# Performance work log

Hardware: AMD Instinct MI355X
Metric: run time of the kernel (lower is better)

Reference implementation:

```python
import jax, jax.numpy as jnp
import numpy as np
import math

B, N, D_IN, D, D_OUT, H = 4, 2048, 128, 128, 256, 4  # D = dim_hidden//2


def _lin(key, din, dout):
    k1, k2 = jax.random.split(key)
    s = 1.0 / math.sqrt(din)
    W = jax.random.uniform(k1, (din, dout), jnp.float32, -s, s)
    b = jax.random.uniform(k2, (dout,), jnp.float32, -s, s)
    return W, b


def setup_inputs() -> dict:
    key = jax.random.key(0)
    ks = jax.random.split(key, 20)
    inp = {"X": jax.random.normal(ks[0], (B, N, D_IN), jnp.float32)}
    # mab dims: (dim_Q, dim_K) -> dim_V=D for each of the 3 MABs
    mab_dims = [(D_IN, D_IN), (D, D), (D, D)]
    ki = 1
    for i, (dq, dk) in enumerate(mab_dims):
        inp[f"m{i}_Wq"], inp[f"m{i}_bq"] = _lin(ks[ki], dq, D); ki += 1
        inp[f"m{i}_Wk"], inp[f"m{i}_bk"] = _lin(ks[ki], dk, D); ki += 1
        inp[f"m{i}_Wv"], inp[f"m{i}_bv"] = _lin(ks[ki], dk, D); ki += 1
        inp[f"m{i}_Wo"], inp[f"m{i}_bo"] = _lin(ks[ki], D, D); ki += 1
    a = math.sqrt(6.0 / (D + 1))  # xavier_uniform for S [1,1,D]
    inp["S"] = jax.random.uniform(ks[ki], (1, 1, D), jnp.float32, -a, a); ki += 1
    inp["pW"], inp["pb"] = _lin(ks[ki], D, D_OUT)
    return inp


def _mab(Q, K, Wq, bq, Wk, bk, Wv, bv, Wo, bo):
    # Linear projections
    Qp = Q @ Wq + bq                       # [B, Nq, D]
    Kp = K @ Wk + bk                       # [B, Nk, D]
    Vp = K @ Wv + bv                       # [B, Nk, D]
    b, nq, dV = Qp.shape
    dh = dV // H
    # torch split(dim_split,2)+cat(0) == head-split on last dim
    Qh = Qp.reshape(b, nq, H, dh)
    Kh = Kp.reshape(b, -1, H, dh)
    Vh = Vp.reshape(b, -1, H, dh)
    # sigmoid attention (no softmax normalizer)
    A = jax.nn.sigmoid(jnp.einsum('bnhd,bmhd->bhnm', Qh, Kh) / jnp.sqrt(jnp.float32(dV)))
    O = Qh + jnp.einsum('bhnm,bmhd->bnhd', A, Vh)
    O = O.reshape(b, nq, dV)
    # residual ReLU-FFN (no LayerNorm since ln=False)
    return O + jax.nn.relu(O @ Wo + bo)


def reference(X,
              m0_Wq, m0_bq, m0_Wk, m0_bk, m0_Wv, m0_bv, m0_Wo, m0_bo,
              m1_Wq, m1_bq, m1_Wk, m1_bk, m1_Wv, m1_bv, m1_Wo, m1_bo,
              m2_Wq, m2_bq, m2_Wk, m2_bk, m2_Wv, m2_bv, m2_Wo, m2_bo,
              S, pW, pb):
    # SAB layer 0: self-attention, dim_in -> D
    Xh = _mab(X, X, m0_Wq, m0_bq, m0_Wk, m0_bk, m0_Wv, m0_bv, m0_Wo, m0_bo)
    # SAB layer 1: D -> D
    Xh = _mab(Xh, Xh, m1_Wq, m1_bq, m1_Wk, m1_bk, m1_Wv, m1_bv, m1_Wo, m1_bo)
    # PMA pooling: seed queries attend over the set
    Sb = jnp.broadcast_to(S, (Xh.shape[0], S.shape[1], S.shape[2]))
    P = _mab(Sb, Xh, m2_Wq, m2_bq, m2_Wk, m2_bk, m2_Wv, m2_bv, m2_Wo, m2_bo)
    # final projection D -> dim_hidden
    return P @ pW + pb  # [B, num_seeds, D_OUT]
```

## Files before the change

kernel.cpp:

```cpp
#include <hip/hip_runtime.h>
#include <hip/hip_bf16.h>

typedef __hip_bfloat16 HB;
typedef __attribute__((ext_vector_type(8))) short short8;
typedef __attribute__((ext_vector_type(4))) short short4v;
typedef __attribute__((ext_vector_type(4))) float f32x4;
typedef __attribute__((ext_vector_type(2))) unsigned int uint2v;
typedef __attribute__((ext_vector_type(4))) unsigned int uint4v;

constexpr int Bn = 4, Nn = 2048, Dm = 128, Hh = 4;
constexpr int MN = Bn * Nn;
constexpr size_t SZ = (size_t)MN * Dm;

static __device__ __forceinline__ short f2bs(float x) {
    __hip_bfloat16 h = __float2bfloat16(x);
    return __builtin_bit_cast(short, h);
}
static __device__ __forceinline__ unsigned short f2bh(float x) {
    return (unsigned short)((__builtin_bit_cast(unsigned int, x) + 0x8000u) >> 16);
}
static __device__ __forceinline__ unsigned int pk2(float lo, float hi) {
    unsigned int a = __builtin_bit_cast(unsigned int, lo) + 0x8000u;
    unsigned int b = __builtin_bit_cast(unsigned int, hi) + 0x8000u;
#if __has_builtin(__builtin_amdgcn_perm)
    return __builtin_amdgcn_perm(b, a, 0x07060302u);
#else
    return (a >> 16) | (b & 0xFFFF0000u);
#endif
}

__global__ void k_wprep(const float* __restrict__ Wa, const float* __restrict__ Wb,
                        const float* __restrict__ Wc, const float* __restrict__ Wd,
                        const float* __restrict__ We, const float* __restrict__ Wf,
                        const float* __restrict__ Wg, const float* __restrict__ Wh,
                        const float* __restrict__ Wi, const float* __restrict__ Wj,
                        HB* __restrict__ WtAll) {
    const float* src;
    switch (blockIdx.x) {
        case 0: src = Wa; break; case 1: src = Wb; break;
        case 2: src = Wc; break; case 3: src = Wd; break;
        case 4: src = We; break; case 5: src = Wf; break;
        case 6: src = Wg; break; case 7: src = Wh; break;
        case 8: src = Wi; break; default: src = Wj; break;
    }
    HB* dst = WtAll + (size_t)blockIdx.x * 16384;
    #pragma unroll
    for (int it = 0; it < 8; ++it) {
        int idx = it * 256 + threadIdx.x;
        int g = idx >> 7, c = idx & 127;
        short8 p;
        #pragma unroll
        for (int j = 0; j < 8; ++j) p[j] = f2bs(src[(size_t)(g * 8 + j) * 128 + c]);
        *(short8*)((short*)dst + (size_t)idx * 8) = p;
    }
}

template<int NW, int RELU, int NEXTRA, int FUSE>
__global__ __launch_bounds__(512) void k_linm(
        const float* __restrict__ A, const float* __restrict__ extra,
        const HB* __restrict__ Wt0, const float* __restrict__ b0,
        const HB* __restrict__ Wt1, const float* __restrict__ b1,
        const HB* __restrict__ Wt2, const float* __restrict__ b2,
        float* __restrict__ C0, float* __restrict__ C1,
        HB* __restrict__ Kb, HB* __restrict__ Vt) {
    const int tid = threadIdx.x;
    const int w = tid >> 6, lane = tid & 63, l15 = lane & 15, quad = lane >> 4;
    const int row0 = blockIdx.x * 32 + (w >> 2) * 16;
    const int cbase = (w & 3) * 32;

    short8 af[4];
    #pragma unroll
    for (int kc = 0; kc < 4; ++kc) {
        const float* ap = A + (size_t)(row0 + l15) * 128 + kc * 32 + quad * 8;
        float4 x0 = *(const float4*)ap;
        float4 x1 = *(const float4*)(ap + 4);
        if (NEXTRA) {
            const float* ep = extra + (size_t)(row0 + l15) * 128 + kc * 32 + quad * 8;
            float4 e0 = *(const float4*)ep, e1 = *(const float4*)(ep + 4);
            x0.x += e0.x; x0.y += e0.y; x0.z += e0.z; x0.w += e0.w;
            x1.x += e1.x; x1.y += e1.y; x1.z += e1.z; x1.w += e1.w;
        }
        uint4v u;
        u[0] = pk2(x0.x, x0.y); u[1] = pk2(x0.z, x0.w);
        u[2] = pk2(x1.x, x1.y); u[3] = pk2(x1.z, x1.w);
        af[kc] = __builtin_bit_cast(short8, u);
    }

    f32x4 zero = {0.f, 0.f, 0.f, 0.f};
    #pragma unroll
    for (int ct = 0; ct < 2; ++ct) {
        const int col = cbase + ct * 16 + l15;
        #pragma unroll
        for (int s = 0; s < NW; ++s) {
            const HB* Wt = (s == 0) ? Wt0 : (s == 1) ? Wt1 : Wt2;
            const float* bs = (s == 0) ? b0 : (s == 1) ? b1 : b2;
            f32x4 acc = zero;
            #pragma unroll
            for (int kc = 0; kc < 4; ++kc) {
                short8 bf = *(const short8*)((const short*)Wt + ((size_t)(kc * 4 + quad) * 128 + col) * 8);
                acc = __builtin_amdgcn_mfma_f32_16x16x32_bf16(af[kc], bf, acc, 0, 0, 0);
            }
            float bb = bs[col];
            if (s == 0 || !FUSE) {
                float* Cs = (s == 0) ? C0 : C1;
                #pragma unroll
                for (int r = 0; r < 4; ++r) {
                    int row = row0 + quad * 4 + r;
                    float v = acc[r] + bb;
                    if (RELU && s == 0) {
                        float st = A[(size_t)row * 128 + col];
                        if (NEXTRA) st += extra[(size_t)row * 128 + col];
                        v = fmaxf(v, 0.f) + st;
                    }
                    Cs[(size_t)row * 128 + col] = v;
                }
            } else if (s == 1) {
                #pragma unroll
                for (int r = 0; r < 4; ++r) {
                    int row = row0 + quad * 4 + r;
                    ((unsigned short*)Kb)[(size_t)row * 128 + col] = f2bh(acc[r] + bb);
                }
            } else {
                int b_ = row0 >> 11;
                int mloc = (row0 + quad * 4) & 2047;
                int slotb = (mloc & ~31) + (((mloc & 15) >> 2) << 3) + (((mloc >> 4) & 1) << 2);
                int h_ = col >> 5, dh = col & 31;
                uint2v pv;
                pv[0] = pk2(acc[0] + bb, acc[1] + bb);
                pv[1] = pk2(acc[2] + bb, acc[3] + bb);
                *(short4v*)((short*)Vt + ((size_t)((b_ * 4 + h_) * 32 + dh)) * 2048 + slotb)
                    = __builtin_bit_cast(short4v, pv);
            }
        }
    }
}

__global__ __launch_bounds__(256) void k_attn3(const float* __restrict__ Qp, const HB* __restrict__ Kbf,
                                               const HB* __restrict__ Vt, float* __restrict__ Opart) {
    const int tid = threadIdx.x;
    const int w = tid >> 6, lane = tid & 63, l15 = lane & 15, quad = lane >> 4;
    const int bh = blockIdx.x >> 6, qg = blockIdx.x & 63;
    const int b = bh >> 2, h = bh & 3;

    __shared__ float ldsacc[4][32][36];

    const float nscale = -0.08838834764831845f;

    short8 aq[2];
    #pragma unroll
    for (int qa = 0; qa < 2; ++qa) {
        const float* qp = Qp + (size_t)(b * Nn + qg * 32 + qa * 16 + l15) * 128 + h * 32 + quad * 8;
        float4 q0 = *(const float4*)qp;
        float4 q1 = *(const float4*)(qp + 4);
        uint4v u;
        u[0] = pk2(q0.x, q0.y); u[1] = pk2(q0.z, q0.w);
        u[2] = pk2(q1.x, q1.y); u[3] = pk2(q1.z, q1.w);
        aq[qa] = __builtin_bit_cast(short8, u);
    }

    f32x4 zero = {0.f, 0.f, 0.f, 0.f};
    f32x4 o[2][2];
    o[0][0] = zero; o[0][1] = zero; o[1][0] = zero; o[1][1] = zero;

    const short* Kb = (const short*)Kbf + (size_t)b * Nn * 128 + h * 32;
    const short* Vb = (const short*)Vt + (size_t)bh * 32 * Nn;

    #pragma unroll 2
    for (int m0 = w * 512; m0 < w * 512 + 512; m0 += 64) {
        short8 kb[4];
        #pragma unroll
        for (int mc = 0; mc < 4; ++mc)
            kb[mc] = *(const short8*)(Kb + (size_t)(m0 + mc * 16 + l15) * 128 + quad * 8);
        short8 vf[2][2];
        #pragma unroll
        for (int t = 0; t < 2; ++t)
            #pragma unroll
            for (int u = 0; u < 2; ++u)
                vf[t][u] = *(const short8*)(Vb + (size_t)(t * 16 + l15) * Nn + m0 + u * 32 + quad * 8);

        #pragma unroll
        for (int qa = 0; qa < 2; ++qa) {
            f32x4 s[4];
            #pragma unroll
            for (int mc = 0; mc < 4; ++mc)
                s[mc] = __builtin_amdgcn_mfma_f32_16x16x32_bf16(kb[mc], aq[qa], zero, 0, 0, 0);
            #pragma unroll
            for (int u = 0; u < 2; ++u) {
                f32x4 lo = s[2 * u], hi = s[2 * u + 1];
                float p0 = __builtin_amdgcn_rcpf(1.f + __expf(lo[0] * nscale));
                float p1 = __builtin_amdgcn_rcpf(1.f + __expf(lo[1] * nscale));
                float p2 = __builtin_amdgcn_rcpf(1.f + __expf(lo[2] * nscale));
                float p3 = __builtin_amdgcn_rcpf(1.f + __expf(lo[3] * nscale));
                float p4 = __builtin_amdgcn_rcpf(1.f + __expf(hi[0] * nscale));
                float p5 = __builtin_amdgcn_rcpf(1.f + __expf(hi[1] * nscale));
                float p6 = __builtin_amdgcn_rcpf(1.f + __expf(hi[2] * nscale));
                float p7 = __builtin_amdgcn_rcpf(1.f + __expf(hi[3] * nscale));
                uint4v pu;
                pu[0] = pk2(p0, p1); pu[1] = pk2(p2, p3);
                pu[2] = pk2(p4, p5); pu[3] = pk2(p6, p7);
                short8 pf = __builtin_bit_cast(short8, pu);
                #pragma unroll
                for (int t = 0; t < 2; ++t)
                    o[qa][t] = __builtin_amdgcn_mfma_f32_16x16x32_bf16(vf[t][u], pf, o[qa][t], 0, 0, 0);
            }
        }
    }

    #pragma unroll
    for (int qa = 0; qa < 2; ++qa)
        #pragma unroll
        for (int t = 0; t < 2; ++t)
            *(f32x4*)&ldsacc[w][qa * 16 + l15][t * 16 + quad * 4] = o[qa][t];
    __syncthreads();
    const int row = tid >> 3, cc = (tid & 7) * 4;
    f32x4 r0 = *(f32x4*)&ldsacc[0][row][cc];
    f32x4 r1 = *(f32x4*)&ldsacc[1][row][cc];
    f32x4 r2 = *(f32x4*)&ldsacc[2][row][cc];
    f32x4 r3 = *(f32x4*)&ldsacc[3][row][cc];
    f32x4 sum = (r0 + r1) + (r2 + r3);
    *(f32x4*)(Opart + (size_t)(b * Nn + qg * 32 + row) * 128 + h * 32 + cc) = sum;
}

__global__ void k_pma2(const float* __restrict__ S, const float* __restrict__ Wq, const float* __restrict__ bq,
                       const float* __restrict__ Kp, const float* __restrict__ Vp,
                       float* __restrict__ P0part) {
    const int bh = blockIdx.x, b = bh >> 2, h = bh & 3;
    const int ms = blockIdx.y;
    const int tid = threadIdx.x;
    __shared__ float4 qs4[8];
    float* qs = (float*)qs4;
    if (tid < 32) {
        float a = bq[h * 32 + tid];
        for (int k = 0; k < 128; ++k)
            a = fmaf(S[k], Wq[k * Dm + h * 32 + tid], a);
        qs[tid] = a;
    }
    __syncthreads();

    float4 q[8];
    #pragma unroll
    for (int i = 0; i < 8; ++i) q[i] = qs4[i];

    const size_t base = (size_t)b * Nn * Dm + h * 32;
    const float nscale = -0.08838834764831845f;
    const int m = ms * 256 + tid;

    const float4* kp = (const float4*)(Kp + base + (size_t)m * Dm);
    const float4* vp = (const float4*)(Vp + base + (size_t)m * Dm);
    float d0 = 0.f, d1 = 0.f, d2 = 0.f, d3 = 0.f;
    #pragma unroll
    for (int c = 0; c < 8; c += 4) {
        float4 k0 = kp[c+0], k1 = kp[c+1], k2 = kp[c+2], k3 = kp[c+3];
        d0 += q[c+0].x*k0.x + q[c+0].y*k0.y + q[c+0].z*k0.z + q[c+0].w*k0.w;
        d1 += q[c+1].x*k1.x + q[c+1].y*k1.y + q[c+1].z*k1.z + q[c+1].w*k1.w;
        d2 += q[c+2].x*k2.x + q[c+2].y*k2.y + q[c+2].z*k2.z + q[c+2].w*k2.w;
        d3 += q[c+3].x*k3.x + q[c+3].y*k3.y + q[c+3].z*k3.z + q[c+3].w*k3.w;
    }
    float dot = (d0 + d1) + (d2 + d3);
    float a = __builtin_amdgcn_rcpf(1.f + __expf(dot * nscale));
    float4 acc[8];
    #pragma unroll
    for (int c = 0; c < 8; ++c) {
        float4 vv = vp[c];
        acc[c].x = a * vv.x; acc[c].y = a * vv.y; acc[c].z = a * vv.z; acc[c].w = a * vv.w;
    }
    #pragma unroll
    for (int off = 1; off < 64; off <<= 1) {
        #pragma unroll
        for (int c = 0; c < 8; ++c) {
            acc[c].x += __shfl_xor(acc[c].x, off);
            acc[c].y += __shfl_xor(acc[c].y, off);
            acc[c].z += __shfl_xor(acc[c].z, off);
            acc[c].w += __shfl_xor(acc[c].w, off);
        }
    }
    __shared__ float red[4][32];
    const int wave = tid >> 6, lane = tid & 63;
    if (lane == 0) {
        #pragma unroll
        for (int c = 0; c < 8; ++c) {
            red[wave][c*4+0] = acc[c].x; red[wave][c*4+1] = acc[c].y;
            red[wave][c*4+2] = acc[c].z; red[wave][c*4+3] = acc[c].w;
        }
    }
    __syncthreads();
    if (tid < 32) {
        float t = (red[0][tid] + red[1][tid]) + (red[2][tid] + red[3][tid]);
        if (ms == 0) t += qs[tid];
        P0part[ms * 512 + b * 128 + h * 32 + tid] = t;
    }
}

__global__ __launch_bounds__(256) void k_lin_small(
                      const float* __restrict__ A,
                      const float* __restrict__ extra, int nextra, int estride,
                      const float* __restrict__ W0, const float* __restrict__ b0,
                      int M, float* __restrict__ C0) {
    __shared__ float ldsf[16 * 128];
    const int tid = threadIdx.x;

    #pragma unroll
    for (int it = 0; it < 2; ++it) {
        int f = it * 256 + tid;
        int r = f >> 5, c = f & 31;
        float4 v = make_float4(0.f, 0.f, 0.f, 0.f);
        if (r < M) {
            v = ((const float4*)(A + (size_t)r * 128))[c];
            for (int e = 0; e < nextra; ++e) {
                float4 w = ((const float4*)(extra + (size_t)e * estride + (size_t)r * 128))[c];
                v.x += w.x; v.y += w.y; v.z += w.z; v.w += w.w;
            }
        }
        ((float4*)ldsf)[f] = v;
    }
    __syncthreads();

    const int col = tid & 127;
    const int rg  = tid >> 7;
    float acc[2] = {0.f, 0.f};
    #pragma unroll 8
    for (int k = 0; k < 128; ++k) {
        float w = W0[k * 128 + col];
        acc[0] = fmaf(ldsf[rg * 128 + k], w, acc[0]);
        acc[1] = fmaf(ldsf[(rg + 2) * 128 + k], w, acc[1]);
    }
    float bb = b0[col];
    #pragma unroll
    for (int i = 0; i < 2; ++i) {
        int r = rg + 2 * i;
        if (r < M) {
            float v = fmaxf(acc[i] + bb, 0.f) + ldsf[r * 128 + col];
            C0[(size_t)r * 128 + col] = v;
        }
    }
}

__global__ void k_final(const float* __restrict__ P, const float* __restrict__ pW,
                        const float* __restrict__ pb, float* __restrict__ out) {
    const int b = blockIdx.x, c = threadIdx.x;
    __shared__ float ps[128];
    if (c < 128) ps[c] = P[b * Dm + c];
    __syncthreads();
    float a = pb[c];
    #pragma unroll 8
    for (int k = 0; k < 128; ++k)
        a = fmaf(ps[k], pW[k * 256 + c], a);
    out[b * 256 + c] = a;
}

extern "C" void kernel_launch(void* const* d_in, const int* in_sizes, int n_in,
                              void* d_out, int out_size, void* d_ws, size_t ws_size,
                              hipStream_t stream) {
    const float* X = (const float*)d_in[0];
    auto W = [&](int i) { return (const float*)d_in[i]; };
    float* ws = (float*)d_ws;

    float* s0 = ws + 0 * SZ;
    float* s1 = ws + 1 * SZ;
    float* s2 = ws + 2 * SZ;
    float* s3 = ws + 3 * SZ;
    HB*    Kbf = (HB*)(ws + 4 * SZ);
    HB*    Vt  = Kbf + SZ;
    HB*    WtAll = (HB*)(ws + 5 * SZ);
    auto Wt = [&](int idx) { return (const HB*)(WtAll + (size_t)idx * 16384); };
    float* P0part = s1;
    float* Pp     = s1 + 8192;

    const int GLM = MN / 32;
    const int attn_blocks = Bn * Hh * (Nn / 32);
    dim3 pma_grid(Bn * Hh, 8);
    const float* nul = nullptr;
    const HB* nulh = nullptr;
    HB* nulhm = nullptr;

    k_wprep<<<10, 256, 0, stream>>>(W(1), W(3), W(5), W(7), W(9), W(11), W(13), W(15),
                                    W(19), W(21), WtAll);

    k_linm<3,0,0,1><<<GLM, 512, 0, stream>>>(X, nul, Wt(0), W(2), Wt(1), W(4), Wt(2), W(6),
                                             s0, nullptr, Kbf, Vt);
    k_attn3<<<attn_blocks, 256, 0, stream>>>(s0, Kbf, Vt, s2);
    k_linm<1,1,1,0><<<GLM, 512, 0, stream>>>(s0, s2, Wt(3), W(8), nulh, nul, nulh, nul,
                                             s1, nullptr, nulhm, nulhm);

    k_linm<3,0,0,1><<<GLM, 512, 0, stream>>>(s1, nul, Wt(4), W(10), Wt(5), W(12), Wt(6), W(14),
                                             s0, nullptr, Kbf, Vt);
    k_attn3<<<attn_blocks, 256, 0, stream>>>(s0, Kbf, Vt, s2);
    k_linm<1,1,1,0><<<GLM, 512, 0, stream>>>(s0, s2, Wt(7), W(16), nulh, nul, nulh, nul,
                                             s3, nullptr, nulhm, nulhm);

    k_linm<2,0,0,0><<<GLM, 512, 0, stream>>>(s3, nul, Wt(8), W(20), Wt(9), W(22), nulh, nul,
                                             s0, s2, nulhm, nulhm);
    k_pma2<<<pma_grid, 256, 0, stream>>>((const float*)d_in[25], W(17), W(18), s0, s2, P0part);
    k_lin_small<<<1, 256, 0, stream>>>(P0part, P0part + 512, 7, 512, W(23), W(24), Bn, Pp);

    k_final<<<Bn, 256, 0, stream>>>(Pp, (const float*)d_in[26], (const float*)d_in[27], (float*)d_out);
}
```

Baseline: 236.7 us.

## Fuse output FFN with next layer's QKV projections and merge tail kernels

```diff
diff --git a/kernel.cpp b/kernel.cpp
--- a/kernel.cpp
+++ b/kernel.cpp
@@ -45,8 +45,8 @@
     }
     HB* dst = WtAll + (size_t)blockIdx.x * 16384;
     #pragma unroll
-    for (int it = 0; it < 8; ++it) {
-        int idx = it * 256 + threadIdx.x;
+    for (int it = 0; it < 2; ++it) {
+        int idx = blockIdx.y * 512 + it * 256 + threadIdx.x;
         int g = idx >> 7, c = idx & 127;
         short8 p;
         #pragma unroll
@@ -135,6 +135,116 @@
     }
 }
 
+template<int NQKV, int FUSE>
+__global__ __launch_bounds__(512) void k_fused(
+        const float* __restrict__ A, const float* __restrict__ extra,
+        const HB* __restrict__ WtO, const float* __restrict__ bO,
+        const HB* __restrict__ Wt0, const float* __restrict__ b0,
+        const HB* __restrict__ Wt1, const float* __restrict__ b1,
+        const HB* __restrict__ Wt2, const float* __restrict__ b2,
+        float* __restrict__ C0, float* __restrict__ C1,
+        HB* __restrict__ Kb, HB* __restrict__ Vt) {
+    const int tid = threadIdx.x;
+    const int w = tid >> 6, lane = tid & 63, l15 = lane & 15, quad = lane >> 4;
+    const int lrow0 = (w >> 2) * 16;
+    const int row0 = blockIdx.x * 32 + lrow0;
+    const int cbase = (w & 3) * 32;
+
+    __shared__ float xs[32 * 132];
+
+    short8 af[4];
+    #pragma unroll
+    for (int kc = 0; kc < 4; ++kc) {
+        const float* ap = A + (size_t)(row0 + l15) * 128 + kc * 32 + quad * 8;
+        float4 x0 = *(const float4*)ap;
+        float4 x1 = *(const float4*)(ap + 4);
+        const float* ep = extra + (size_t)(row0 + l15) * 128 + kc * 32 + quad * 8;
+        float4 e0 = *(const float4*)ep, e1 = *(const float4*)(ep + 4);
+        x0.x += e0.x; x0.y += e0.y; x0.z += e0.z; x0.w += e0.w;
+        x1.x += e1.x; x1.y += e1.y; x1.z += e1.z; x1.w += e1.w;
+        uint4v u;
+        u[0] = pk2(x0.x, x0.y); u[1] = pk2(x0.z, x0.w);
+        u[2] = pk2(x1.x, x1.y); u[3] = pk2(x1.z, x1.w);
+        af[kc] = __builtin_bit_cast(short8, u);
+    }
+
+    f32x4 zero = {0.f, 0.f, 0.f, 0.f};
+
+    #pragma unroll
+    for (int ct = 0; ct < 2; ++ct) {
+        const int col = cbase + ct * 16 + l15;
+        f32x4 acc = zero;
+        #pragma unroll
+        for (int kc = 0; kc < 4; ++kc) {
+            short8 bf = *(const short8*)((const short*)WtO + ((size_t)(kc * 4 + quad) * 128 + col) * 8);
+            acc = __builtin_amdgcn_mfma_f32_16x16x32_bf16(af[kc], bf, acc, 0, 0, 0);
+        }
+        float bb = bO[col];
+        #pragma unroll
+        for (int r = 0; r < 4; ++r) {
+            int row = row0 + quad * 4 + r;
+            float st = A[(size_t)row * 128 + col] + extra[(size_t)row * 128 + col];
+            xs[(lrow0 + quad * 4 + r) * 132 + col] = fmaxf(acc[r] + bb, 0.f) + st;
+        }
+    }
+    __syncthreads();
+
+    short8 a2[4];
+    {
+        const float* xrow = xs + (size_t)(lrow0 + l15) * 132;
+        #pragma unroll
+        for (int kc = 0; kc < 4; ++kc) {
+            f32x4 x0 = *(const f32x4*)(xrow + kc * 32 + quad * 8);
+            f32x4 x1 = *(const f32x4*)(xrow + kc * 32 + quad * 8 + 4);
+            uint4v u;
+            u[0] = pk2(x0[0], x0[1]); u[1] = pk2(x0[2], x0[3]);
+            u[2] = pk2(x1[0], x1[1]); u[3] = pk2(x1[2], x1[3]);
+            a2[kc] = __builtin_bit_cast(short8, u);
+        }
+    }
+
+    #pragma unroll
+    for (int ct = 0; ct < 2; ++ct) {
+        const int col = cbase + ct * 16 + l15;
+        #pragma unroll
+        for (int s = 0; s < NQKV; ++s) {
+            const HB* Wt = (s == 0) ? Wt0 : (s == 1) ? Wt1 : Wt2;
+            const float* bs = (s == 0) ? b0 : (s == 1) ? b1 : b2;
+            f32x4 acc = zero;
+            #pragma unroll
+            for (int kc = 0; kc < 4; ++kc) {
+                short8 bf = *(const short8*)((const short*)Wt + ((size_t)(kc * 4 + quad) * 128 + col) * 8);
+                acc = __builtin_amdgcn_mfma_f32_16x16x32_bf16(a2[kc], bf, acc, 0, 0, 0);
+            }
+            float bb = bs[col];
+            if (s == 0 || !FUSE) {
+                float* Cs = (s == 0) ? C0 : C1;
+                #pragma unroll
+                for (int r = 0; r < 4; ++r) {
+                    int row = row0 + quad * 4 + r;
+                    Cs[(size_t)row * 128 + col] = acc[r] + bb;
+                }
+            } else if (s == 1) {
+                #pragma unroll
+                for (int r = 0; r < 4; ++r) {
+                    int row = row0 + quad * 4 + r;
+                    ((unsigned short*)Kb)[(size_t)row * 128 + col] = f2bh(acc[r] + bb);
+                }
+            } else {
+                int b_ = row0 >> 11;
+                int mloc = (row0 + quad * 4) & 2047;
+                int slotb = (mloc & ~31) + (((mloc & 15) >> 2) << 3) + (((mloc >> 4) & 1) << 2);
+                int h_ = col >> 5, dh = col & 31;
+                uint2v pv;
+                pv[0] = pk2(acc[0] + bb, acc[1] + bb);
+                pv[1] = pk2(acc[2] + bb, acc[3] + bb);
+                *(short4v*)((short*)Vt + ((size_t)((b_ * 4 + h_) * 32 + dh)) * 2048 + slotb)
+                    = __builtin_bit_cast(short4v, pv);
+            }
+        }
+    }
+}
+
 __global__ __launch_bounds__(256) void k_attn3(const float* __restrict__ Qp, const HB* __restrict__ Kbf,
                                                const HB* __restrict__ Vt, float* __restrict__ Opart) {
     const int tid = threadIdx.x;
@@ -291,61 +401,32 @@
     }
 }
 
-__global__ __launch_bounds__(256) void k_lin_small(
-                      const float* __restrict__ A,
-                      const float* __restrict__ extra, int nextra, int estride,
-                      const float* __restrict__ W0, const float* __restrict__ b0,
-                      int M, float* __restrict__ C0) {
-    __shared__ float ldsf[16 * 128];
-    const int tid = threadIdx.x;
-
-    #pragma unroll
-    for (int it = 0; it < 2; ++it) {
-        int f = it * 256 + tid;
-        int r = f >> 5, c = f & 31;
-        float4 v = make_float4(0.f, 0.f, 0.f, 0.f);
-        if (r < M) {
-            v = ((const float4*)(A + (size_t)r * 128))[c];
-            for (int e = 0; e < nextra; ++e) {
-                float4 w = ((const float4*)(extra + (size_t)e * estride + (size_t)r * 128))[c];
-                v.x += w.x; v.y += w.y; v.z += w.z; v.w += w.w;
-            }
-        }
-        ((float4*)ldsf)[f] = v;
-    }
-    __syncthreads();
-
-    const int col = tid & 127;
-    const int rg  = tid >> 7;
-    float acc[2] = {0.f, 0.f};
-    #pragma unroll 8
-    for (int k = 0; k < 128; ++k) {
-        float w = W0[k * 128 + col];
-        acc[0] = fmaf(ldsf[rg * 128 + k], w, acc[0]);
-        acc[1] = fmaf(ldsf[(rg + 2) * 128 + k], w, acc[1]);
-    }
-    float bb = b0[col];
-    #pragma unroll
-    for (int i = 0; i < 2; ++i) {
-        int r = rg + 2 * i;
-        if (r < M) {
-            float v = fmaxf(acc[i] + bb, 0.f) + ldsf[r * 128 + col];
-            C0[(size_t)r * 128 + col] = v;
-        }
-    }
-}
-
-__global__ void k_final(const float* __restrict__ P, const float* __restrict__ pW,
-                        const float* __restrict__ pb, float* __restrict__ out) {
-    const int b = blockIdx.x, c = threadIdx.x;
-    __shared__ float ps[128];
-    if (c < 128) ps[c] = P[b * Dm + c];
-    __syncthreads();
-    float a = pb[c];
+__global__ __launch_bounds__(256) void k_tail(const float* __restrict__ P0part,
+                                              const float* __restrict__ W23, const float* __restrict__ b23,
+                                              const float* __restrict__ pW, const float* __restrict__ pb,
+                                              float* __restrict__ out) {
+    const int b = blockIdx.x, tid = threadIdx.x;
+    __shared__ float staged[128], pp[128];
+    if (tid < 128) {
+        float s = 0.f;
+        #pragma unroll
+        for (int ms = 0; ms < 8; ++ms) s += P0part[ms * 512 + b * 128 + tid];
+        staged[tid] = s;
+    }
+    __syncthreads();
+    if (tid < 128) {
+        float acc = b23[tid];
+        #pragma unroll 8
+        for (int k = 0; k < 128; ++k)
+            acc = fmaf(staged[k], W23[k * 128 + tid], acc);
+        pp[tid] = fmaxf(acc, 0.f) + staged[tid];
+    }
+    __syncthreads();
+    float a = pb[tid];
     #pragma unroll 8
     for (int k = 0; k < 128; ++k)
-        a = fmaf(ps[k], pW[k * 256 + c], a);
-    out[b * 256 + c] = a;
+        a = fmaf(pp[k], pW[k * 256 + tid], a);
+    out[b * 256 + tid] = a;
 }
 
 extern "C" void kernel_launch(void* const* d_in, const int* in_sizes, int n_in,
@@ -364,34 +445,30 @@
     HB*    WtAll = (HB*)(ws + 5 * SZ);
     auto Wt = [&](int idx) { return (const HB*)(WtAll + (size_t)idx * 16384); };
     float* P0part = s1;
-    float* Pp     = s1 + 8192;
 
     const int GLM = MN / 32;
     const int attn_blocks = Bn * Hh * (Nn / 32);
+    dim3 wprep_grid(10, 4);
     dim3 pma_grid(Bn * Hh, 8);
     const float* nul = nullptr;
-    const HB* nulh = nullptr;
-    HB* nulhm = nullptr;
-
-    k_wprep<<<10, 256, 0, stream>>>(W(1), W(3), W(5), W(7), W(9), W(11), W(13), W(15),
-                                    W(19), W(21), WtAll);
+
+    k_wprep<<<wprep_grid, 256, 0, stream>>>(W(1), W(3), W(5), W(7), W(9), W(11), W(13), W(15),
+                                            W(19), W(21), WtAll);
 
     k_linm<3,0,0,1><<<GLM, 512, 0, stream>>>(X, nul, Wt(0), W(2), Wt(1), W(4), Wt(2), W(6),
                                              s0, nullptr, Kbf, Vt);
     k_attn3<<<attn_blocks, 256, 0, stream>>>(s0, Kbf, Vt, s2);
-    k_linm<1,1,1,0><<<GLM, 512, 0, stream>>>(s0, s2, Wt(3), W(8), nulh, nul, nulh, nul,
-                                             s1, nullptr, nulhm, nulhm);
-
-    k_linm<3,0,0,1><<<GLM, 512, 0, stream>>>(s1, nul, Wt(4), W(10), Wt(5), W(12), Wt(6), W(14),
-                                             s0, nullptr, Kbf, Vt);
-    k_attn3<<<attn_blocks, 256, 0, stream>>>(s0, Kbf, Vt, s2);
-    k_linm<1,1,1,0><<<GLM, 512, 0, stream>>>(s0, s2, Wt(7), W(16), nulh, nul, nulh, nul,
-                                             s3, nullptr, nulhm, nulhm);
-
-    k_linm<2,0,0,0><<<GLM, 512, 0, stream>>>(s3, nul, Wt(8), W(20), Wt(9), W(22), nulh, nul,
-                                             s0, s2, nulhm, nulhm);
-    k_pma2<<<pma_grid, 256, 0, stream>>>((const float*)d_in[25], W(17), W(18), s0, s2, P0part);
-    k_lin_small<<<1, 256, 0, stream>>>(P0part, P0part + 512, 7, 512, W(23), W(24), Bn, Pp);
-
-    k_final<<<Bn, 256, 0, stream>>>(Pp, (const float*)d_in[26], (const float*)d_in[27], (float*)d_out);
-}
+
+    k_fused<3,1><<<GLM, 512, 0, stream>>>(s0, s2, Wt(3), W(8),
+                                          Wt(4), W(10), Wt(5), W(12), Wt(6), W(14),
+                                          s1, nullptr, Kbf, Vt);
+    k_attn3<<<attn_blocks, 256, 0, stream>>>(s1, Kbf, Vt, s2);
+
+    k_fused<2,0><<<GLM, 512, 0, stream>>>(s1, s2, Wt(7), W(16),
+                                          Wt(8), W(20), Wt(9), W(22), nullptr, nul,
+                                          s0, s3, nullptr, nullptr);
+
+    k_pma2<<<pma_grid, 256, 0, stream>>>((const float*)d_in[25], W(17), W(18), s0, s3, P0part);
+    k_tail<<<Bn, 256, 0, stream>>>(P0part, W(23), W(24), (const float*)d_in[26], (const float*)d_in[27],
+                                   (float*)d_out);
+}
```

Result: faster. 227.5 us (-3.9%).
